# Optimization experiments

Hardware: AMD Instinct MI355X
Metric: run time of the kernel (lower is better)

The kernel has to match this reference:

```python
import jax, jax.numpy as jnp
import numpy as np

K = 3          # deformable conv kernel size
PAD = 1        # padding
BN_EPS = 1e-5


def _upsample2(x):
    # nn.Upsample(scale_factor=2) default mode='nearest' on [B,C,D,H,W]
    x = jnp.repeat(x, 2, axis=2)
    x = jnp.repeat(x, 2, axis=3)
    x = jnp.repeat(x, 2, axis=4)
    return x


def _conv3d(x, w, b):
    out = jax.lax.conv_general_dilated(
        x, w, window_strides=(1, 1, 1), padding=[(PAD, PAD)] * 3,
        dimension_numbers=('NCDHW', 'OIDHW', 'NCDHW'))
    return out + b[None, :, None, None, None]


def _trilinear_sample(x, coords):
    # x: [B,C,D,H,W]; coords: [B,Kt,3,D,H,W] absolute (possibly OOB) positions.
    # Zero padding outside the volume (standard deformable-conv convention).
    B, C, D, H, W = x.shape
    pd, ph, pw = coords[:, :, 0], coords[:, :, 1], coords[:, :, 2]  # [B,Kt,D,H,W]
    d0 = jnp.floor(pd); h0 = jnp.floor(ph); w0 = jnp.floor(pw)
    fd = pd - d0; fh = ph - h0; fw = pw - w0
    x_flat = x.reshape(B, C, D * H * W)

    def gather(di, hi, wi):
        valid = ((di >= 0) & (di < D) & (hi >= 0) & (hi < H) & (wi >= 0) & (wi < W))
        dc = jnp.clip(di, 0, D - 1).astype(jnp.int32)
        hc = jnp.clip(hi, 0, H - 1).astype(jnp.int32)
        wc = jnp.clip(wi, 0, W - 1).astype(jnp.int32)
        flat = (dc * H + hc) * W + wc                       # [B,Kt,D,H,W]
        vals = jax.vmap(lambda xf, idx: jnp.take(xf, idx.reshape(-1), axis=1))(x_flat, flat)
        vals = vals.reshape(B, C, *flat.shape[1:])          # [B,C,Kt,D,H,W]
        return vals * valid[:, None].astype(x.dtype)

    out = jnp.zeros((B, C) + pd.shape[1:], x.dtype)
    for dd in (0, 1):
        for hh in (0, 1):
            for ww in (0, 1):
                wgt = ((fd if dd else 1.0 - fd)
                       * (fh if hh else 1.0 - fh)
                       * (fw if ww else 1.0 - fw))           # [B,Kt,D,H,W]
                out = out + gather(d0 + dd, h0 + hh, w0 + ww) * wgt[:, None]
    return out  # [B,C,Kt,D,H,W]


def _deform_conv3d(x, w_off, b_off, w, b):
    B, C, D, H, W = x.shape
    Kt = K ** 3
    # offsets: Conv3d(C, 3*K^3, k=3, pad=1) -> [B, Kt, 3(dz,dy,dx), D,H,W]
    off = _conv3d(x, w_off, b_off).reshape(B, Kt, 3, D, H, W)
    # kernel tap displacements relative to output voxel: [Kt,3]
    taps = jnp.stack(jnp.meshgrid(jnp.arange(K), jnp.arange(K), jnp.arange(K),
                                  indexing='ij'), -1).reshape(-1, 3).astype(x.dtype) - PAD
    grid = jnp.stack(jnp.meshgrid(jnp.arange(D, dtype=x.dtype),
                                  jnp.arange(H, dtype=x.dtype),
                                  jnp.arange(W, dtype=x.dtype),
                                  indexing='ij'), 0)          # [3,D,H,W]
    coords = grid[None, None] + taps[None, :, :, None, None, None] + off  # [B,Kt,3,D,H,W]
    sampled = _trilinear_sample(x, coords)                    # [B,C,Kt,D,H,W]
    out = jnp.einsum('bckdhw,ock->bodhw', sampled, w.reshape(w.shape[0], C, Kt))
    return out + b[None, :, None, None, None]


def setup_inputs() -> dict:
    key = jax.random.key(0)
    ks = jax.random.split(key, 4)
    ch_in, ch_out = 64, 32
    x = jax.random.normal(ks[0], (1, ch_in, 16, 16, 16), jnp.float32)
    w_off = jax.random.normal(ks[1], (3 * K ** 3, ch_in, K, K, K), jnp.float32) * 0.01
    b_off = jnp.zeros((3 * K ** 3,), jnp.float32)
    w = jax.random.normal(ks[2], (ch_out, ch_in, K, K, K), jnp.float32) * 0.05
    b = jnp.zeros((ch_out,), jnp.float32)
    gamma = jnp.ones((ch_out,), jnp.float32)
    beta = jnp.zeros((ch_out,), jnp.float32)
    return {"x": x, "w_off": w_off, "b_off": b_off, "w": w, "b": b,
            "gamma": gamma, "beta": beta}


def reference(x, w_off, b_off, w, b, gamma, beta):
    x = _upsample2(x)                                  # [B,C,2D,2H,2W]
    out = _deform_conv3d(x, w_off, b_off, w, b)        # [B,ch_out,2D,2H,2W]
    # BatchNorm3d (training-mode batch stats) + ReLU
    mean = out.mean(axis=(0, 2, 3, 4), keepdims=True)
    var = out.var(axis=(0, 2, 3, 4), keepdims=True)
    out = (out - mean) * jax.lax.rsqrt(var + BN_EPS)
    out = out * gamma[None, :, None, None, None] + beta[None, :, None, None, None]
    return jax.nn.relu(out)
```

## Files before the change

kernel.cpp:

```cpp
#include <hip/hip_runtime.h>
#include <math.h>

#define NVOX  32768
#define CIN   64
#define COUT  32
#define KT    27
#define CIT   1728
#define PSP   5832

#define WS_XT   0
#define WS_WA   186624
#define WS_W2   214272
#define WS_STAT 412928

typedef __attribute__((ext_vector_type(8))) _Float16 half8;
typedef __attribute__((ext_vector_type(2))) _Float16 half2v;
typedef __attribute__((ext_vector_type(4))) float floatx4;

static __device__ __forceinline__ unsigned dup16(float w) {
    unsigned short b = __builtin_bit_cast(unsigned short, (_Float16)w);
    return (unsigned)b * 0x10001u;
}
static __device__ __forceinline__ half2v u2h2(unsigned u) {
    return __builtin_bit_cast(half2v, u);
}
static __device__ __forceinline__ half8 pk8(half2v a, half2v b, half2v c, half2v d) {
    union { half8 v; half2v p[4]; } u;
    u.p[0] = a; u.p[1] = b; u.p[2] = c; u.p[3] = d;
    return u.v;
}

__global__ __launch_bounds__(256) void prep_all_kernel(
        const float* __restrict__ x, const float* __restrict__ w_off,
        const float* __restrict__ wmat, float* __restrict__ ws) {
    int b = blockIdx.x, t = threadIdx.x;
    if (b < 92) {
        __shared__ _Float16 tile[64][65];
        _Float16* xth = (_Float16*)(ws + WS_XT);
        int tq = t >> 6, lane = t & 63;
        int base = b * 64;
        int cell = base + lane;
        int qw = cell % 18, qh = (cell / 18) % 18, qd = cell / 324;
        bool interior = (cell < PSP) && qd >= 1 && qd <= 16 && qh >= 1 && qh <= 16
                        && qw >= 1 && qw <= 16;
        int xbase = interior ? (((qd - 1) * 16 + (qh - 1)) * 16 + (qw - 1)) : 0;
#pragma unroll
        for (int i = 0; i < 16; i++) {
            int c = tq * 16 + i;
            float v = interior ? x[c * 4096 + xbase] : 0.f;
            tile[lane][c] = (_Float16)v;
        }
        __syncthreads();
#pragma unroll
        for (int i = 0; i < 16; i++) {
            int s = tq * 16 + i;
            int cell2 = base + s;
            if (cell2 < PSP) xth[cell2 * 64 + lane] = tile[s][lane];
        }
    } else if (b < 119) {
        _Float16* wa = (_Float16*)(ws + WS_WA);
        int idx = (b - 92) * 256 + t;
        int kb = idx >> 5, o = idx & 31;
        half8 r;
#pragma unroll
        for (int j = 0; j < 8; j++) {
            int kk = kb * 8 + j;
            int tap = kk >> 6, ci = kk & 63;
            r[j] = (_Float16)wmat[o * CIT + ci * 27 + tap];
        }
        *(half8*)(wa + idx * 8) = r;
    } else if (b < 311) {
        _Float16* w2 = (_Float16*)(ws + WS_W2);
        int idx = (b - 119) * 256 + t;
        int pi = idx / 6144;
        int rem = idx - pi * 6144;
        int kb = rem / 96, m = rem - (rem / 96) * 96;
        int pid = pi >> 2, pih = (pi >> 1) & 1, piw = pi & 1;
        half8 r;
#pragma unroll
        for (int j = 0; j < 8; j++) {
            int kk = kb * 8 + j;
            int tap2 = kk >> 6, ci = kk & 63;
            int cd = tap2 >> 2, ch = (tap2 >> 1) & 1, cw = tap2 & 1;
            int bd = pid ? (cd ? 2 : 0) : cd;
            int nd = pid ? (cd ? 1 : 2) : (cd ? 2 : 1);
            int bh = pih ? (ch ? 2 : 0) : ch;
            int nh = pih ? (ch ? 1 : 2) : (ch ? 2 : 1);
            int bw = piw ? (cw ? 2 : 0) : cw;
            int nw = piw ? (cw ? 1 : 2) : (cw ? 2 : 1);
            float s = 0.f;
            if (m < 81) {
                const float* wp = w_off + (m * 64 + ci) * 27;
                for (int a = 0; a < nd; a++)
                    for (int bb = 0; bb < nh; bb++)
                        for (int c = 0; c < nw; c++)
                            s += wp[(bd + a) * 9 + (bh + bb) * 3 + (bw + c)];
            }
            r[j] = (_Float16)s;
        }
        int widx = pi * 6208 + (kb >> 3) * 776 + (kb & 7) * 97 + m;
        *(half8*)(w2 + widx * 8) = r;
    } else {
        if (t < 64) ws[WS_STAT + t] = 0.f;
    }
}

#define ACCP(xl, xh, Wx) do { \
    s00 += (Wx) * u2h2((unsigned)(xl).x); s01 += (Wx) * u2h2((unsigned)(xl).y); \
    s02 += (Wx) * u2h2((unsigned)(xl).z); s03 += (Wx) * u2h2((unsigned)(xl).w); \
    s10 += (Wx) * u2h2((unsigned)(xh).x); s11 += (Wx) * u2h2((unsigned)(xh).y); \
    s12 += (Wx) * u2h2((unsigned)(xh).z); s13 += (Wx) * u2h2((unsigned)(xh).w); \
} while (0)

#define DO2(ap, wp) do { \
    int a0_ = (ap) & 0x7fff, a1_ = (int)((((unsigned)(ap)) >> 16) & 0x7fffu); \
    unsigned wl_ = ((unsigned)(wp) & 0xffffu) * 0x10001u; \
    unsigned wh_ = (((unsigned)(wp)) >> 16) * 0x10001u; \
    int4 x0l_ = *(const int4*)(region + a0_ + subLo); \
    int4 x0h_ = *(const int4*)(region + a0_ + subHi); \
    int4 x1l_ = *(const int4*)(region + a1_ + subLo); \
    int4 x1h_ = *(const int4*)(region + a1_ + subHi); \
    ACCP(x0l_, x0h_, u2h2(wl_)); ACCP(x1l_, x1h_, u2h2(wh_)); \
} while (0)

#define GSLOW(Ax, wf) do { \
    half2v Wq_ = u2h2(dup16(wf)); \
    int4 xl_ = *(const int4*)(xtb + (Ax) + subLo); \
    int4 xh_ = *(const int4*)(xtb + (Ax) + subLo + 64); \
    t00 += Wq_ * u2h2((unsigned)xl_.x); t01 += Wq_ * u2h2((unsigned)xl_.y); \
    t02 += Wq_ * u2h2((unsigned)xl_.z); t03 += Wq_ * u2h2((unsigned)xl_.w); \
    t10 += Wq_ * u2h2((unsigned)xh_.x); t11 += Wq_ * u2h2((unsigned)xh_.y); \
    t12 += Wq_ * u2h2((unsigned)xh_.z); t13 += Wq_ * u2h2((unsigned)xh_.w); \
} while (0)

__global__ __launch_bounds__(256, 4) void fused_kernel(
        const float* __restrict__ b_off, const float* __restrict__ bias,
        float* ws, float* __restrict__ out) {
    __shared__ __align__(16) char shmem[37376];
    char* region = shmem;
    int2* scratch2 = (int2*)(shmem + 28160);
    _Float16* Pl = (_Float16*)(shmem + 31232);
    float* pbuf = (float*)shmem;
    float* rsumS = (float*)(shmem + 8704);
    float* rsqS  = (float*)(shmem + 8832);

    int tid = threadIdx.x, wave = tid >> 6, lane = tid & 63;
    int col = lane & 15, quad = lane >> 4;
    int bid = blockIdx.x;
    int pi = bid >> 7, tile = bid & 127;
    int pid = pi >> 2, pih = (pi >> 1) & 1, piw = pi & 1;
    int qd0 = (tile >> 4) << 1;
    int qh0 = ((tile >> 1) & 7) << 1;
    int qw0 = (tile & 1) << 3;

    const char* xtb = (const char*)(ws + WS_XT);
    const half8* wa8 = (const half8*)(ws + WS_WA);
    float* gstat = ws + WS_STAT;

    {
        int4* ab4 = (int4*)shmem;
        const _Float16* abuf16 = (const _Float16*)shmem;
        const int4* wsrc = (const int4*)(ws + WS_W2) + pi * 6208;
        int nsub = wave & 1, kh = wave >> 1;
        int vv = nsub * 16 + col;
        int qdv = qd0 + (vv >> 4), qhv = qh0 + ((vv >> 3) & 1), qwv = qw0 + (vv & 7);

        int4 bx[8];
#pragma unroll
        for (int tap = 0; tap < 8; tap++) {
            int cd = tap >> 2, ch = (tap >> 1) & 1, cw = tap & 1;
            int cell = ((qdv + cd + pid) * 18 + (qhv + ch + pih)) * 18 + (qwv + cw + piw);
            bx[tap] = *(const int4*)(xtb + cell * 128 + kh * 64 + quad * 16);
        }

        int4 ra0 = wsrc[tid], ra1 = wsrc[256 + tid], ra2 = wsrc[512 + tid];
        int4 ra3 = (tid < 8) ? wsrc[768 + tid] : make_int4(0, 0, 0, 0);
        ab4[tid] = ra0; ab4[256 + tid] = ra1; ab4[512 + tid] = ra2;
        if (tid < 8) ab4[768 + tid] = ra3;
        ra0 = wsrc[776 + tid]; ra1 = wsrc[776 + 256 + tid]; ra2 = wsrc[776 + 512 + tid];
        if (tid < 8) ra3 = wsrc[776 + 768 + tid];
        __syncthreads();

        floatx4 acc[6];
#pragma unroll
        for (int mt = 0; mt < 6; mt++) acc[mt] = (floatx4){0.f, 0.f, 0.f, 0.f};

        int fb = (kh * 4 + quad) * 776 + col * 8;

#pragma unroll
        for (int tap = 0; tap < 8; tap++) {
            if (tap < 7) {
                int4* dst = ab4 + ((tap + 1) & 1) * 776;
                dst[tid] = ra0; dst[256 + tid] = ra1; dst[512 + tid] = ra2;
                if (tid < 8) dst[768 + tid] = ra3;
            }
            if (tap < 6) {
                const int4* s2 = wsrc + (tap + 2) * 776;
                ra0 = s2[tid]; ra1 = s2[256 + tid]; ra2 = s2[512 + tid];
                if (tid < 8) ra3 = s2[768 + tid];
            }
            half8 bfrag = __builtin_bit_cast(half8, bx[tap]);
            const _Float16* abh = abuf16 + (tap & 1) * 6208;
#pragma unroll
            for (int mt = 0; mt < 6; mt++) {
                half8 af = *(const half8*)(abh + fb + mt * 128);
                acc[mt] = __builtin_amdgcn_mfma_f32_16x16x32_f16(af, bfrag, acc[mt], 0, 0, 0);
            }
            __syncthreads();
        }

        float* red = (float*)shmem;
        if (kh == 1) {
#pragma unroll
            for (int mt = 0; mt < 6; mt++)
#pragma unroll
                for (int r = 0; r < 4; r++)
                    red[(nsub * 96 + mt * 16 + quad * 4 + r) * 17 + col] = acc[mt][r];
        }
        __syncthreads();
        if (kh == 0) {
#pragma unroll
            for (int mt = 0; mt < 6; mt++)
#pragma unroll
                for (int r = 0; r < 4; r++) {
                    int m = mt * 16 + quad * 4 + r;
                    if (m < 81)
                        Pl[m * 32 + vv] = (_Float16)(acc[mt][r]
                                         + red[(nsub * 96 + m) * 17 + col] + b_off[m]);
                }
        }
        __syncthreads();
    }

#pragma unroll 1
    for (int it = 0; it < 5; it++) {
        int i = it * 256 + tid;
        int r = i >> 3, c16 = i & 7;
        int rd = r / 40, rem = r - rd * 40, rh = rem / 10, rw = rem - rh * 10;
        int cell = ((qd0 + rd) * 18 + (qh0 + rh)) * 18 + (qw0 + rw);
        int4 vsrc = *(const int4*)(xtb + cell * 128 + c16 * 16);
        *(int4*)(region + r * 176 + c16 * 16) = vsrc;
    }
    __syncthreads();

    int vh = wave & 1, kt = wave >> 1;
    int v = vh * 16 + col;
    int qdv = qd0 + (v >> 4), qhv = qh0 + ((v >> 3) & 1), qwv = qw0 + (v & 7);
    int dcoord = 2 * qdv + pid, hcoord = 2 * qhv + pih, wcoord = 2 * qwv + piw;
    int gvox = dcoord * 1024 + hcoord * 32 + wcoord;
    int tbeg = kt ? 14 : 0, tend = kt ? 27 : 14;
    int subLo = quad * 16, subHi = subLo + 64;
    int bd = quad >> 1, bh = quad & 1;

    floatx4 acc0 = {0.f, 0.f, 0.f, 0.f}, acc1 = {0.f, 0.f, 0.f, 0.f};

    float od = (float)Pl[(3 * tbeg + 0) * 32 + v];
    float oh = (float)Pl[(3 * tbeg + 1) * 32 + v];
    float ow = (float)Pl[(3 * tbeg + 2) * 32 + v];

#pragma unroll 1
    for (int tap = tbeg; tap < tend; tap++) {
        int kd = tap / 9, r9 = tap - kd * 9, kh2 = r9 / 3, kw2 = r9 - kh2 * 3;
        float pdc = (float)(dcoord + kd - 1) + od;
        float phc = (float)(hcoord + kh2 - 1) + oh;
        float pwc = (float)(wcoord + kw2 - 1) + ow;
        float fd0 = floorf(pdc), fh0 = floorf(phc), fw0 = floorf(pwc);
        float fd = pdc - fd0, fh = phc - fh0, fw = pwc - fw0;
        int id = (int)fd0, ih = (int)fh0, iw = (int)fw0;

        int cd0 = ((min(max(id,     -2), 33)) >> 1) + 1;
        int cd1 = ((min(max(id + 1, -2), 33)) >> 1) + 1;
        int ch0 = ((min(max(ih,     -2), 33)) >> 1) + 1;
        int ch1 = ((min(max(ih + 1, -2), 33)) >> 1) + 1;
        int cw0 = ((min(max(iw,     -2), 33)) >> 1) + 1;
        int cw1 = ((min(max(iw + 1, -2), 33)) >> 1) + 1;
        int sd0 = cd0 - qd0, sd1 = cd1 - qd0;
        int sh0 = ch0 - qh0, sh1 = ch1 - qh0;
        int sw0 = cw0 - qw0, sw1 = cw1 - qw0;
        bool oob = ((unsigned)sd0 > 3u) | ((unsigned)sd1 > 3u)
                 | ((unsigned)sh0 > 3u) | ((unsigned)sh1 > 3u)
                 | ((unsigned)sw0 > 9u) | ((unsigned)sw1 > 9u);

        int sdq = bd ? sd1 : sd0, shq = bh ? sh1 : sh0;
        int rb = (sdq * 4 + shq) * 10;
        int r0 = rb + sw0, r1 = rb + sw1;
        int a0 = oob ? 0x8000 : (r0 * 176);
        int a1 = oob ? 0x8000 : (r1 * 176);
        float gdw = 1.f - fd, ghw = 1.f - fh, gww = 1.f - fw;
        float wd = bd ? fd : gdw, wh = bh ? fh : ghw;
        float wdh = wd * wh;
        unsigned wb0 = (unsigned)__builtin_bit_cast(unsigned short, (_Float16)(wdh * gww));
        unsigned wb1 = (unsigned)__builtin_bit_cast(unsigned short, (_Float16)(wdh * fw));
        scratch2[(wave * 16 + col) * 6 + quad] =
            make_int2(a0 | (a1 << 16), (int)(wb0 | (wb1 << 16)));

        if (tap + 1 < tend) {
            od = (float)Pl[(3 * tap + 3) * 32 + v];
            oh = (float)Pl[(3 * tap + 4) * 32 + v];
            ow = (float)Pl[(3 * tap + 5) * 32 + v];
        }

        int kb = tap * 8 + quad;
        half8 a00 = wa8[kb * 32 + col];
        half8 a01 = wa8[kb * 32 + 16 + col];
        half8 a10 = wa8[(kb + 4) * 32 + col];
        half8 a11 = wa8[(kb + 4) * 32 + 16 + col];

        const int4* sc = (const int4*)(scratch2 + (wave * 16 + col) * 6);
        int4 p0 = sc[0], p1 = sc[1];

        half2v s00 = {0, 0}, s01 = {0, 0}, s02 = {0, 0}, s03 = {0, 0};
        half2v s10 = {0, 0}, s11 = {0, 0}, s12 = {0, 0}, s13 = {0, 0};
        DO2(p0.x, p0.y); DO2(p0.z, p0.w);
        DO2(p1.x, p1.y); DO2(p1.z, p1.w);

        if (__any((p0.x & 0x8000) != 0)) {
            bool flg = (p0.x & 0x8000) != 0;
            int Rd0 = ((min(max(id,     -2), 33) >> 1) + 1) * (324 * 128);
            int Rd1 = ((min(max(id + 1, -2), 33) >> 1) + 1) * (324 * 128);
            int Rh0 = ((min(max(ih,     -2), 33) >> 1) + 1) * (18 * 128);
            int Rh1 = ((min(max(ih + 1, -2), 33) >> 1) + 1) * (18 * 128);
            int Rw0 = ((min(max(iw,     -2), 33) >> 1) + 1) * 128;
            int Rw1 = ((min(max(iw + 1, -2), 33) >> 1) + 1) * 128;
            half2v t00 = {0,0}, t01 = {0,0}, t02 = {0,0}, t03 = {0,0};
            half2v t10 = {0,0}, t11 = {0,0}, t12 = {0,0}, t13 = {0,0};
            GSLOW(Rd0 + Rh0 + Rw0, gdw * ghw * gww);
            GSLOW(Rd0 + Rh0 + Rw1, gdw * ghw * fw);
            GSLOW(Rd0 + Rh1 + Rw0, gdw * fh  * gww);
            GSLOW(Rd0 + Rh1 + Rw1, gdw * fh  * fw);
            GSLOW(Rd1 + Rh0 + Rw0, fd  * ghw * gww);
            GSLOW(Rd1 + Rh0 + Rw1, fd  * ghw * fw);
            GSLOW(Rd1 + Rh1 + Rw0, fd  * fh  * gww);
            GSLOW(Rd1 + Rh1 + Rw1, fd  * fh  * fw);
            s00 = flg ? t00 : s00; s01 = flg ? t01 : s01;
            s02 = flg ? t02 : s02; s03 = flg ? t03 : s03;
            s10 = flg ? t10 : s10; s11 = flg ? t11 : s11;
            s12 = flg ? t12 : s12; s13 = flg ? t13 : s13;
        }

        half8 bf0 = pk8(s00, s01, s02, s03);
        half8 bf1 = pk8(s10, s11, s12, s13);

        acc0 = __builtin_amdgcn_mfma_f32_16x16x32_f16(a00, bf0, acc0, 0, 0, 0);
        acc1 = __builtin_amdgcn_mfma_f32_16x16x32_f16(a01, bf0, acc1, 0, 0, 0);
        acc0 = __builtin_amdgcn_mfma_f32_16x16x32_f16(a10, bf1, acc0, 0, 0, 0);
        acc1 = __builtin_amdgcn_mfma_f32_16x16x32_f16(a11, bf1, acc1, 0, 0, 0);
    }

    __syncthreads();
    if (kt == 1) {
#pragma unroll
        for (int r = 0; r < 4; r++) {
            pbuf[((vh * 2 + 0) * 16 + quad * 4 + r) * 17 + col] = acc0[r];
            pbuf[((vh * 2 + 1) * 16 + quad * 4 + r) * 17 + col] = acc1[r];
        }
    }
    if (tid < 64) ((float*)(shmem + 8704))[tid] = 0.f;
    __syncthreads();
    if (kt == 0) {
#pragma unroll
        for (int r = 0; r < 4; r++) {
            int i = quad * 4 + r;
            int o0 = i;
            float v0 = acc0[r] + pbuf[((vh * 2 + 0) * 16 + i) * 17 + col] + bias[o0];
            out[o0 * NVOX + gvox] = v0;
            atomicAdd(&rsumS[o0], v0);
            atomicAdd(&rsqS[o0], v0 * v0);
            int o1 = 16 + i;
            float v1 = acc1[r] + pbuf[((vh * 2 + 1) * 16 + i) * 17 + col] + bias[o1];
            out[o1 * NVOX + gvox] = v1;
            atomicAdd(&rsumS[o1], v1);
            atomicAdd(&rsqS[o1], v1 * v1);
        }
    }
    __syncthreads();
    if (tid < COUT) {
        atomicAdd(&gstat[tid], rsumS[tid]);
        atomicAdd(&gstat[COUT + tid], rsqS[tid]);
    }
}

__global__ void bn_kernel(const float* __restrict__ ws,
                          const float* __restrict__ gamma,
                          const float* __restrict__ beta,
                          float* out) {
    int i = blockIdx.x * 256 + threadIdx.x;
    int o = i >> 13;
    const float* gstat = ws + WS_STAT;
    const float inv = 1.f / 32768.f;
    float mean = gstat[o] * inv;
    float var  = gstat[COUT + o] * inv - mean * mean;
    float sc   = rsqrtf(var + 1e-5f) * gamma[o];
    float bt   = beta[o];
    float4 v = ((float4*)out)[i];
    v.x = fmaxf((v.x - mean) * sc + bt, 0.f);
    v.y = fmaxf((v.y - mean) * sc + bt, 0.f);
    v.z = fmaxf((v.z - mean) * sc + bt, 0.f);
    v.w = fmaxf((v.w - mean) * sc + bt, 0.f);
    ((float4*)out)[i] = v;
}

extern "C" void kernel_launch(void* const* d_in, const int* in_sizes, int n_in,
                              void* d_out, int out_size, void* d_ws, size_t ws_size,
                              hipStream_t stream) {
    const float* x     = (const float*)d_in[0];
    const float* w_off = (const float*)d_in[1];
    const float* b_off = (const float*)d_in[2];
    const float* wmat  = (const float*)d_in[3];
    const float* bias  = (const float*)d_in[4];
    const float* gamma = (const float*)d_in[5];
    const float* beta  = (const float*)d_in[6];
    float* ws  = (float*)d_ws;
    float* out = (float*)d_out;

    prep_all_kernel<<<312, 256, 0, stream>>>(x, w_off, wmat, ws);
    fused_kernel<<<1024, 256, 0, stream>>>(b_off, bias, ws, out);
    bn_kernel<<<1024, 256, 0, stream>>>(ws, gamma, beta, out);
}
```

Before: 134.8 us.

## Double fused kernel block size to 512 threads, splitting offset and tap work

The fused kernel now runs 8 waves per block instead of 4. In the offset-conv phase the M dimension is split between wave halves, and the per-tap B fragments are prefetched one step ahead instead of all eight being loaded up front. In the deformable-sampling phase the 27 taps are split four ways instead of two, and three partial accumulators are reduced through shared memory. The aim is more latency hiding and less serial work per wave, at the cost of larger shared memory, more reduction traffic and possibly lower occupancy under the 512-thread launch bound.

```diff
diff --git a/kernel.cpp b/kernel.cpp
--- a/kernel.cpp
+++ b/kernel.cpp
@@ -133,16 +133,16 @@
     t12 += Wq_ * u2h2((unsigned)xh_.z); t13 += Wq_ * u2h2((unsigned)xh_.w); \
 } while (0)
 
-__global__ __launch_bounds__(256, 4) void fused_kernel(
+__global__ __launch_bounds__(512, 8) void fused_kernel(
         const float* __restrict__ b_off, const float* __restrict__ bias,
         float* ws, float* __restrict__ out) {
-    __shared__ __align__(16) char shmem[37376];
+    __shared__ __align__(16) char shmem[40448];
     char* region = shmem;
     int2* scratch2 = (int2*)(shmem + 28160);
-    _Float16* Pl = (_Float16*)(shmem + 31232);
+    _Float16* Pl = (_Float16*)(shmem + 34304);
     float* pbuf = (float*)shmem;
-    float* rsumS = (float*)(shmem + 8704);
-    float* rsqS  = (float*)(shmem + 8832);
+    float* rsumS = (float*)(shmem + 16384);
+    float* rsqS  = (float*)(shmem + 16512);
 
     int tid = threadIdx.x, wave = tid >> 6, lane = tid & 63;
     int col = lane & 15, quad = lane >> 4;
@@ -161,85 +161,93 @@
         int4* ab4 = (int4*)shmem;
         const _Float16* abuf16 = (const _Float16*)shmem;
         const int4* wsrc = (const int4*)(ws + WS_W2) + pi * 6208;
-        int nsub = wave & 1, kh = wave >> 1;
+        int nsub = wave & 1, kh = (wave >> 1) & 1, mh = wave >> 2;
         int vv = nsub * 16 + col;
         int qdv = qd0 + (vv >> 4), qhv = qh0 + ((vv >> 3) & 1), qwv = qw0 + (vv & 7);
 
-        int4 bx[8];
-#pragma unroll
-        for (int tap = 0; tap < 8; tap++) {
-            int cd = tap >> 2, ch = (tap >> 1) & 1, cw = tap & 1;
-            int cell = ((qdv + cd + pid) * 18 + (qhv + ch + pih)) * 18 + (qwv + cw + piw);
-            bx[tap] = *(const int4*)(xtb + cell * 128 + kh * 64 + quad * 16);
-        }
-
-        int4 ra0 = wsrc[tid], ra1 = wsrc[256 + tid], ra2 = wsrc[512 + tid];
-        int4 ra3 = (tid < 8) ? wsrc[768 + tid] : make_int4(0, 0, 0, 0);
-        ab4[tid] = ra0; ab4[256 + tid] = ra1; ab4[512 + tid] = ra2;
-        if (tid < 8) ab4[768 + tid] = ra3;
-        ra0 = wsrc[776 + tid]; ra1 = wsrc[776 + 256 + tid]; ra2 = wsrc[776 + 512 + tid];
-        if (tid < 8) ra3 = wsrc[776 + 768 + tid];
+        int c0 = ((qdv + pid) * 18 + (qhv + pih)) * 18 + (qwv + piw);
+        int4 bxc = *(const int4*)(xtb + c0 * 128 + kh * 64 + quad * 16);
+
+        int4 ra0 = wsrc[tid];
+        int4 ra1 = (tid < 264) ? wsrc[512 + tid] : make_int4(0, 0, 0, 0);
+        ab4[tid] = ra0;
+        if (tid < 264) ab4[512 + tid] = ra1;
+        ra0 = wsrc[776 + tid];
+        if (tid < 264) ra1 = wsrc[776 + 512 + tid];
         __syncthreads();
 
-        floatx4 acc[6];
-#pragma unroll
-        for (int mt = 0; mt < 6; mt++) acc[mt] = (floatx4){0.f, 0.f, 0.f, 0.f};
-
-        int fb = (kh * 4 + quad) * 776 + col * 8;
+        floatx4 acc[3];
+#pragma unroll
+        for (int mt = 0; mt < 3; mt++) acc[mt] = (floatx4){0.f, 0.f, 0.f, 0.f};
+
+        int fb = (kh * 4 + quad) * 776 + (mh * 48 + col) * 8;
 
 #pragma unroll
         for (int tap = 0; tap < 8; tap++) {
             if (tap < 7) {
                 int4* dst = ab4 + ((tap + 1) & 1) * 776;
-                dst[tid] = ra0; dst[256 + tid] = ra1; dst[512 + tid] = ra2;
-                if (tid < 8) dst[768 + tid] = ra3;
+                dst[tid] = ra0;
+                if (tid < 264) dst[512 + tid] = ra1;
             }
             if (tap < 6) {
                 const int4* s2 = wsrc + (tap + 2) * 776;
-                ra0 = s2[tid]; ra1 = s2[256 + tid]; ra2 = s2[512 + tid];
-                if (tid < 8) ra3 = s2[768 + tid];
+                ra0 = s2[tid];
+                if (tid < 264) ra1 = s2[512 + tid];
             }
-            half8 bfrag = __builtin_bit_cast(half8, bx[tap]);
+            int4 bxn = bxc;
+            if (tap < 7) {
+                int tn = tap + 1;
+                int cd = tn >> 2, ch = (tn >> 1) & 1, cw = tn & 1;
+                int cell = ((qdv + cd + pid) * 18 + (qhv + ch + pih)) * 18
+                         + (qwv + cw + piw);
+                bxn = *(const int4*)(xtb + cell * 128 + kh * 64 + quad * 16);
+            }
+            half8 bfrag = __builtin_bit_cast(half8, bxc);
             const _Float16* abh = abuf16 + (tap & 1) * 6208;
 #pragma unroll
-            for (int mt = 0; mt < 6; mt++) {
+            for (int mt = 0; mt < 3; mt++) {
                 half8 af = *(const half8*)(abh + fb + mt * 128);
                 acc[mt] = __builtin_amdgcn_mfma_f32_16x16x32_f16(af, bfrag, acc[mt], 0, 0, 0);
             }
+            bxc = bxn;
             __syncthreads();
         }
 
         float* red = (float*)shmem;
         if (kh == 1) {
 #pragma unroll
-            for (int mt = 0; mt < 6; mt++)
+            for (int mt = 0; mt < 3; mt++)
 #pragma unroll
                 for (int r = 0; r < 4; r++)
-                    red[(nsub * 96 + mt * 16 + quad * 4 + r) * 17 + col] = acc[mt][r];
+                    red[(((mh * 2 + nsub) * 48) + mt * 16 + quad * 4 + r) * 17 + col]
+                        = acc[mt][r];
         }
         __syncthreads();
         if (kh == 0) {
 #pragma unroll
-            for (int mt = 0; mt < 6; mt++)
+            for (int mt = 0; mt < 3; mt++)
 #pragma unroll
                 for (int r = 0; r < 4; r++) {
-                    int m = mt * 16 + quad * 4 + r;
+                    int mrow = mt * 16 + quad * 4 + r;
+                    int m = mh * 48 + mrow;
                     if (m < 81)
                         Pl[m * 32 + vv] = (_Float16)(acc[mt][r]
-                                         + red[(nsub * 96 + m) * 17 + col] + b_off[m]);
+                            + red[(((mh * 2 + nsub) * 48) + mrow) * 17 + col] + b_off[m]);
                 }
         }
         __syncthreads();
     }
 
 #pragma unroll 1
-    for (int it = 0; it < 5; it++) {
-        int i = it * 256 + tid;
-        int r = i >> 3, c16 = i & 7;
-        int rd = r / 40, rem = r - rd * 40, rh = rem / 10, rw = rem - rh * 10;
-        int cell = ((qd0 + rd) * 18 + (qh0 + rh)) * 18 + (qw0 + rw);
-        int4 vsrc = *(const int4*)(xtb + cell * 128 + c16 * 16);
-        *(int4*)(region + r * 176 + c16 * 16) = vsrc;
+    for (int it = 0; it < 3; it++) {
+        int i = it * 512 + tid;
+        if (i < 1280) {
+            int r = i >> 3, c16 = i & 7;
+            int rd = r / 40, rem = r - rd * 40, rh = rem / 10, rw = rem - rh * 10;
+            int cell = ((qd0 + rd) * 18 + (qh0 + rh)) * 18 + (qw0 + rw);
+            int4 vsrc = *(const int4*)(xtb + cell * 128 + c16 * 16);
+            *(int4*)(region + r * 176 + c16 * 16) = vsrc;
+        }
     }
     __syncthreads();
 
@@ -248,7 +256,7 @@
     int qdv = qd0 + (v >> 4), qhv = qh0 + ((v >> 3) & 1), qwv = qw0 + (v & 7);
     int dcoord = 2 * qdv + pid, hcoord = 2 * qhv + pih, wcoord = 2 * qwv + piw;
     int gvox = dcoord * 1024 + hcoord * 32 + wcoord;
-    int tbeg = kt ? 14 : 0, tend = kt ? 27 : 14;
+    int tbeg = kt * 7, tend = min(27, kt * 7 + 7);
     int subLo = quad * 16, subHi = subLo + 64;
     int bd = quad >> 1, bh = quad & 1;
 
@@ -348,26 +356,33 @@
     }
 
     __syncthreads();
-    if (kt == 1) {
+    if (kt > 0) {
 #pragma unroll
         for (int r = 0; r < 4; r++) {
-            pbuf[((vh * 2 + 0) * 16 + quad * 4 + r) * 17 + col] = acc0[r];
-            pbuf[((vh * 2 + 1) * 16 + quad * 4 + r) * 17 + col] = acc1[r];
-        }
-    }
-    if (tid < 64) ((float*)(shmem + 8704))[tid] = 0.f;
+            int i = quad * 4 + r;
+            pbuf[(((vh * 2 + 0) * 3 + (kt - 1)) * 16 + i) * 17 + col] = acc0[r];
+            pbuf[(((vh * 2 + 1) * 3 + (kt - 1)) * 16 + i) * 17 + col] = acc1[r];
+        }
+    }
+    if (tid < 64) ((float*)(shmem + 16384))[tid] = 0.f;
     __syncthreads();
     if (kt == 0) {
 #pragma unroll
         for (int r = 0; r < 4; r++) {
             int i = quad * 4 + r;
             int o0 = i;
-            float v0 = acc0[r] + pbuf[((vh * 2 + 0) * 16 + i) * 17 + col] + bias[o0];
+            float v0 = acc0[r]
+                     + pbuf[(((vh * 2 + 0) * 3 + 0) * 16 + i) * 17 + col]
+                     + pbuf[(((vh * 2 + 0) * 3 + 1) * 16 + i) * 17 + col]
+                     + pbuf[(((vh * 2 + 0) * 3 + 2) * 16 + i) * 17 + col] + bias[o0];
             out[o0 * NVOX + gvox] = v0;
             atomicAdd(&rsumS[o0], v0);
             atomicAdd(&rsqS[o0], v0 * v0);
             int o1 = 16 + i;
-            float v1 = acc1[r] + pbuf[((vh * 2 + 1) * 16 + i) * 17 + col] + bias[o1];
+            float v1 = acc1[r]
+                     + pbuf[(((vh * 2 + 1) * 3 + 0) * 16 + i) * 17 + col]
+                     + pbuf[(((vh * 2 + 1) * 3 + 1) * 16 + i) * 17 + col]
+                     + pbuf[(((vh * 2 + 1) * 3 + 2) * 16 + i) * 17 + col] + bias[o1];
             out[o1 * NVOX + gvox] = v1;
             atomicAdd(&rsumS[o1], v1);
             atomicAdd(&rsqS[o1], v1 * v1);
@@ -414,6 +429,6 @@
     float* out = (float*)d_out;
 
     prep_all_kernel<<<312, 256, 0, stream>>>(x, w_off, wmat, ws);
-    fused_kernel<<<1024, 256, 0, stream>>>(b_off, bias, ws, out);
+    fused_kernel<<<1024, 512, 0, stream>>>(b_off, bias, ws, out);
     bn_kernel<<<1024, 256, 0, stream>>>(ws, gamma, beta, out);
 }
```

New measurement: 199.2 us. 47.8% more time.
